# Performance work log

Measured on AMD Instinct MI355X. Metric: run time of the kernel, lower is better.

## Reference

```python
import jax, jax.numpy as jnp
import numpy as np

N = 5000        # n_stocks (nodes)
F = 128         # n_features
H = 4           # attention heads
C = 32          # hidden_size per head
HC = H * C      # GAT output dim = GRU input dim
GH = 256        # gru_hidden_size
E = 320000      # directed edges (before self-loops)
NEG_SLOPE = 0.2 # GATv2Conv default leaky_relu slope


def setup_inputs() -> dict:
    key = jax.random.key(0)
    ks = jax.random.split(key, 16)
    s = 0.05
    return {
        "x": jax.random.normal(ks[0], (N, F), dtype=jnp.float32),
        "edge_index": jax.random.randint(ks[1], (2, E), 0, N, dtype=jnp.int64),
        # GATv2Conv params (lin_l, lin_r with bias, attention vector, output bias)
        "W_l": jax.random.normal(ks[2], (F, HC), dtype=jnp.float32) * s,
        "b_l": jax.random.normal(ks[3], (HC,), dtype=jnp.float32) * s,
        "W_r": jax.random.normal(ks[4], (F, HC), dtype=jnp.float32) * s,
        "b_r": jax.random.normal(ks[5], (HC,), dtype=jnp.float32) * s,
        "att": jax.random.normal(ks[6], (H, C), dtype=jnp.float32) * s,
        "gat_bias": jax.random.normal(ks[7], (HC,), dtype=jnp.float32) * s,
        # GRU params (single layer, PyTorch gate order r,z,n)
        "W_ih": jax.random.normal(ks[8], (3 * GH, HC), dtype=jnp.float32) * s,
        "W_hh": jax.random.normal(ks[9], (3 * GH, GH), dtype=jnp.float32) * s,
        "b_ih": jax.random.normal(ks[10], (3 * GH,), dtype=jnp.float32) * s,
        "b_hh": jax.random.normal(ks[11], (3 * GH,), dtype=jnp.float32) * s,
        # policy head + log_std param
        "Wp": jax.random.normal(ks[12], (N, GH), dtype=jnp.float32) * s,
        "bp": jax.random.normal(ks[13], (N,), dtype=jnp.float32) * s,
        "log_std": jnp.zeros((N,), dtype=jnp.float32),
    }


def reference(x, edge_index, W_l, b_l, W_r, b_r, att, gat_bias,
              W_ih, W_hh, b_ih, b_hh, Wp, bp, log_std):
    # --- GATv2Conv (add_self_loops=True, concat heads, eval mode -> no dropout) ---
    loop = jnp.arange(N, dtype=edge_index.dtype)
    src = jnp.concatenate([edge_index[0], loop])  # message source j
    dst = jnp.concatenate([edge_index[1], loop])  # message target i

    xl = (x @ W_l + b_l).reshape(N, H, C)  # source-side transform
    xr = (x @ W_r + b_r).reshape(N, H, C)  # target-side transform

    m = xl[src] + xr[dst]                                  # [Etot, H, C]
    e = jnp.einsum('ehc,hc->eh', jax.nn.leaky_relu(m, NEG_SLOPE), att)

    # segment softmax over incoming edges per target node
    emax = jax.ops.segment_max(e, dst, num_segments=N)      # [N, H]
    ex = jnp.exp(e - emax[dst])
    denom = jax.ops.segment_sum(ex, dst, num_segments=N)    # [N, H]
    alpha = ex / denom[dst]                                 # [Etot, H]

    agg = jax.ops.segment_sum(alpha[:, :, None] * xl[src], dst, num_segments=N)
    gat_out = agg.reshape(N, HC) + gat_bias                 # [N, H*C]

    # --- GRU: each node = one batch element, seq_len=1, h0 = 0 ---
    gi = gat_out @ W_ih.T + b_ih                            # [N, 3*GH]
    gr, gz, gn = jnp.split(gi, 3, axis=1)
    hr, hz, hn = jnp.split(b_hh, 3)                          # h0=0 -> only hh bias
    r = jax.nn.sigmoid(gr + hr)
    z = jax.nn.sigmoid(gz + hz)
    n = jnp.tanh(gn + r * hn)
    h = (1.0 - z) * n                                        # [N, GH]

    # --- policy head ---
    mean = h @ Wp.T + bp                                     # [N, N]
    std = jnp.exp(jnp.clip(log_std, -10.0, 2.0))             # [N]
    return mean, std
```

## Files before the change

### kernel.cpp

```cpp
#include <hip/hip_runtime.h>
#include <hip/hip_bf16.h>
#include <float.h>

#define N_NODES 5000
#define F_IN    128
#define HC      128
#define GH      256
#define NE      320000
#define NET     325000
#define MPAD    5120
#define CAP     160
#define LIN_BLKS   313
#define DEC_BLKS  1270
#define NTHR    (DEC_BLKS * 256)

typedef __bf16 bf16;
typedef __attribute__((ext_vector_type(4))) __bf16 bf16x4;
typedef __attribute__((ext_vector_type(8))) __bf16 bf16x8;
typedef __attribute__((ext_vector_type(4))) float  f32x4;

__device__ __forceinline__ float lrelu(float v) { return v > 0.f ? v : 0.2f * v; }
__device__ __forceinline__ float sigm(float v) { return 1.f / (1.f + __expf(-v)); }

__device__ __forceinline__ void gload16(const void* g, void* l) {
  __builtin_amdgcn_global_load_lds((const __attribute__((address_space(1))) void*)g,
                                   (__attribute__((address_space(3))) void*)l, 16, 0, 0);
}

__global__ void k_init(int* __restrict__ cnt) {
  int i = blockIdx.x * 256 + threadIdx.x;
  if (i < N_NODES) cnt[i] = 0;
}

#define NWIH (768 * HC)
#define NWP  (N_NODES * GH)
__global__ __launch_bounds__(256) void k_pre(
    const float* __restrict__ x,
    const float* __restrict__ Wl, const float* __restrict__ bl,
    const float* __restrict__ Wr, const float* __restrict__ br,
    bf16* __restrict__ xlb, bf16* __restrict__ xrb,
    const float* __restrict__ lstd, float* __restrict__ out_std,
    const int* __restrict__ ei, int* __restrict__ cnt, int* __restrict__ csr_s,
    const float* __restrict__ wih, const float* __restrict__ wp,
    bf16* __restrict__ wihb, bf16* __restrict__ wpb) {
  __shared__ float xs[16][F_IN];
  int t = threadIdx.x;
  if (blockIdx.x < LIN_BLKS) {
    int nb = blockIdx.x * 16;
#pragma unroll
    for (int p = 0; p < 8; ++p) {
      int idx = p * 256 + t;
      int nl = idx >> 7, c = idx & 127;
      int gn = nb + nl;
      xs[nl][c] = (gn < N_NODES) ? x[(size_t)gn * F_IN + c] : 0.f;
    }
    __syncthreads();
    int col = t & 127;
    const float* W = (t < 128) ? Wl : Wr;
    float bias = (t < 128) ? bl[col] : br[col];
    float acc[16];
#pragma unroll
    for (int m = 0; m < 16; ++m) acc[m] = bias;
#pragma unroll 4
    for (int k = 0; k < F_IN; ++k) {
      float w = W[k * HC + col];
#pragma unroll
      for (int m = 0; m < 16; ++m) acc[m] = fmaf(xs[m][k], w, acc[m]);
    }
    bf16* out = (t < 128) ? xlb : xrb;
#pragma unroll
    for (int m = 0; m < 16; ++m) {
      int gn = nb + m;
      if (gn < N_NODES) out[(size_t)gn * HC + col] = (bf16)acc[m];
    }
    if (t < 16) {
      int gn = nb + t;
      if (gn < N_NODES) out_std[gn] = expf(fminf(fmaxf(lstd[gn], -10.f), 2.f));
    }
    return;
  }
  __shared__ int mode;
  if (t == 0) {
    int f = 0;
    for (int q = 1; q < 128; q += 2) f |= ei[q];
    mode = (f == 0) ? 1 : 0;
  }
  __syncthreads();
  int e = (blockIdx.x - LIN_BLKS) * 256 + t;
  for (int i = e; i < NWIH / 4; i += NTHR) {
    float4 v = reinterpret_cast<const float4*>(wih)[i];
    bf16x4 o = {(bf16)v.x, (bf16)v.y, (bf16)v.z, (bf16)v.w};
    *reinterpret_cast<bf16x4*>(&wihb[i * 4]) = o;
  }
  for (int i = e; i < NWP / 4; i += NTHR) {
    float4 v = reinterpret_cast<const float4*>(wp)[i];
    bf16x4 o = {(bf16)v.x, (bf16)v.y, (bf16)v.z, (bf16)v.w};
    *reinterpret_cast<bf16x4*>(&wpb[i * 4]) = o;
  }
  if (e >= NET) return;
  int s, d;
  if (e >= NE) { s = d = e - NE; }
  else if (mode) {
    int2 sv = *reinterpret_cast<const int2*>(&ei[2 * e]);
    int2 dv = *reinterpret_cast<const int2*>(&ei[2 * (NE + e)]);
    s = sv.x; d = dv.x;
  } else { s = ei[e]; d = ei[NE + e]; }
  int slot = atomicAdd(&cnt[d], 1);
  if (slot < CAP) csr_s[d * CAP + slot] = s;
}

__global__ __launch_bounds__(256) void k_gat(
    const bf16* __restrict__ xlb, const bf16* __restrict__ xrb,
    const int* __restrict__ csr_s, const int* __restrict__ cnt,
    const float* __restrict__ att, const float* __restrict__ gbias,
    bf16* __restrict__ gat_b) {
  int t = threadIdx.x;
  int lane = t & 63;
  int node = blockIdx.x * 4 + (t >> 6);
  if (node >= N_NODES) return;
  int c8 = lane & 15;
  int eg = lane >> 4;
  bf16x8 xr8 = *reinterpret_cast<const bf16x8*>(xrb + (size_t)node * HC + c8 * 8);
  float4 w0 = reinterpret_cast<const float4*>(att)[c8 * 2];
  float4 w1 = reinterpret_cast<const float4*>(att)[c8 * 2 + 1];
  float xr[8], wv[8];
#pragma unroll
  for (int k = 0; k < 8; ++k) xr[k] = (float)xr8[k];
  wv[0] = w0.x; wv[1] = w0.y; wv[2] = w0.z; wv[3] = w0.w;
  wv[4] = w1.x; wv[5] = w1.y; wv[6] = w1.z; wv[7] = w1.w;

  float acc[8] = {0.f, 0.f, 0.f, 0.f, 0.f, 0.f, 0.f, 0.f};
  float den = 0.f;
  int deg = cnt[node];
  deg = deg < CAP ? deg : CAP;
  int beg = node * CAP, end = node * CAP + deg;
#pragma unroll 2
  for (int p0 = beg; p0 < end; p0 += 4) {
    int p = p0 + eg;
    bool valid = p < end;
    int j = valid ? csr_s[p] : node;
    bf16x8 a8 = *reinterpret_cast<const bf16x8*>(xlb + (size_t)j * HC + c8 * 8);
    float av[8];
    float tt = 0.f;
#pragma unroll
    for (int k = 0; k < 8; ++k) {
      av[k] = (float)a8[k];
      tt = fmaf(lrelu(av[k] + xr[k]), wv[k], tt);
    }
    tt += __shfl_xor(tt, 1);
    tt += __shfl_xor(tt, 2);
    float pe = valid ? __expf(tt) : 0.f;
    den += pe;
#pragma unroll
    for (int k = 0; k < 8; ++k) acc[k] = fmaf(pe, av[k], acc[k]);
  }
#pragma unroll
  for (int m = 16; m <= 32; m <<= 1) {
    den += __shfl_xor(den, m);
#pragma unroll
    for (int k = 0; k < 8; ++k) acc[k] += __shfl_xor(acc[k], m);
  }
  if (eg == 0) {
    float4 g0 = reinterpret_cast<const float4*>(gbias)[c8 * 2];
    float4 g1 = reinterpret_cast<const float4*>(gbias)[c8 * 2 + 1];
    float gb[8] = {g0.x, g0.y, g0.z, g0.w, g1.x, g1.y, g1.z, g1.w};
    float rden = 1.f / den;
    bf16x8 o;
#pragma unroll
    for (int k = 0; k < 8; ++k) o[k] = (bf16)(acc[k] * rden + gb[k]);
    *reinterpret_cast<bf16x8*>(gat_b + (size_t)node * HC + c8 * 8) = o;
  }
}

__global__ __launch_bounds__(256) void k_gemm_gru(
    const bf16* __restrict__ A, const bf16* __restrict__ wihb,
    const float* __restrict__ bih, const float* __restrict__ bhh,
    bf16* __restrict__ hb) {
  __shared__ char smem[73728];
  char* Ab = smem;
  int t = threadIdx.x;
  int lane = t & 63, wave = t >> 6;
  int wm = wave >> 1, wn = wave & 1;
  int r16 = lane & 15, kg = lane >> 4;
  int sw7 = r16 & 7;
  int bm = blockIdx.x >> 1, bn = blockIdx.x & 1;
  int r0 = bm * 32, c0 = bn * 128;

#pragma unroll
  for (int q = 0; q < 2; ++q) {
    int idx = q * 256 + t;
    int half = idx >> 8, ih = idx & 255;
    int row = ih >> 3, cc = ih & 7;
    int gc = cc ^ (row & 7);
    gload16(&A[(size_t)(r0 + row) * 128 + half * 64 + gc * 8],
            Ab + (q * 256 + wave * 64) * 16);
  }

  auto STAGE_B = [&](int gate, int buf) {
    char* Bb = smem + 8192 + buf * 32768;
#pragma unroll
    for (int q = 0; q < 8; ++q) {
      int idx = q * 256 + t;
      int half = idx >> 10, ih = idx & 1023;
      int row = ih >> 3, cc = ih & 7;
      int gc = cc ^ (row & 7);
      gload16(&wihb[(size_t)(gate * 256 + c0 + row) * 128 + half * 64 + gc * 8],
              Bb + (q * 256 + wave * 64) * 16);
    }
  };

  int rowA = (wm * 16 + r16) * 128;
  int rowB[4];
#pragma unroll
  for (int n = 0; n < 4; ++n) rowB[n] = (wn * 64 + n * 16 + r16) * 128;

  f32x4 acc[3][4] = {};
  STAGE_B(0, 0);
  __syncthreads();
#pragma unroll
  for (int g = 0; g < 3; ++g) {
    if (g < 2) STAGE_B(g + 1, (g + 1) & 1);
    const char* Bb = smem + 8192 + (g & 1) * 32768;
#pragma unroll
    for (int h = 0; h < 2; ++h)
#pragma unroll
      for (int w = 0; w < 2; ++w) {
        int ch = ((w * 4 + kg) ^ sw7) * 16;
        bf16x8 af = *reinterpret_cast<const bf16x8*>(Ab + h * 4096 + rowA + ch);
        bf16x8 bfr[4];
#pragma unroll
        for (int n = 0; n < 4; ++n)
          bfr[n] = *reinterpret_cast<const bf16x8*>(Bb + h * 16384 + rowB[n] + ch);
#pragma unroll
        for (int n = 0; n < 4; ++n)
          acc[g][n] = __builtin_amdgcn_mfma_f32_16x16x32_bf16(af, bfr[n], acc[g][n], 0, 0, 0);
      }
    __syncthreads();
  }

  bf16* hl = (bf16*)Ab;
#pragma unroll
  for (int n = 0; n < 4; ++n) {
    int c = c0 + wn * 64 + n * 16 + r16;
    float bihr = bih[c],       bhhr = bhh[c];
    float bihz = bih[256 + c], bhhz = bhh[256 + c];
    float bihn = bih[512 + c], bhhn = bhh[512 + c];
#pragma unroll
    for (int rr = 0; rr < 4; ++rr) {
      float rg = sigm(acc[0][n][rr] + bihr + bhhr);
      float zg = sigm(acc[1][n][rr] + bihz + bhhz);
      float ng = tanhf(acc[2][n][rr] + bihn + rg * bhhn);
      float hv = (1.f - zg) * ng;
      int row = wm * 16 + kg * 4 + rr;
      hl[row * 128 + (wn * 64 + n * 16 + r16)] = (bf16)hv;
    }
  }
  __syncthreads();
#pragma unroll
  for (int q = 0; q < 2; ++q) {
    int idx = q * 256 + t;
    int row = idx >> 4, cc = idx & 15;
    *reinterpret_cast<int4*>(&hb[(size_t)(r0 + row) * GH + c0 + cc * 8]) =
        *reinterpret_cast<const int4*>(&hl[row * 128 + cc * 8]);
  }
}

__global__ __launch_bounds__(256) void gemm_nt_f32out(
    const bf16* __restrict__ A, const bf16* __restrict__ B,
    const float* __restrict__ bias, float* __restrict__ Cout,
    int K, int ldc, int Mstore, int Nstore, int nbx) {
  __shared__ char smem[65536];
  int t = threadIdx.x;
  int lane = t & 63, wave = t >> 6;
  int wm = wave >> 1, wn = wave & 1;
  int r16 = lane & 15, kg = lane >> 4;

  int wg = blockIdx.x;
  int xcd = wg & 7, i = wg >> 3;
  int bm0 = (xcd * 5 + i % 5) * 128;
  int bn0 = (i / 5) * 128;

  int rsub = lane >> 3;
  int cchk = lane & 7;

  auto STAGE = [&](int buf, int k0) {
    char* Ab = smem + buf * 32768;
#pragma unroll
    for (int q = 0; q < 4; ++q) {
      int row = (wave * 4 + q) * 8 + rsub;
      int gc = cchk ^ (row & 7);
      char* db = Ab + (wave * 4 + q) * 1024;
      gload16(&A[(size_t)(bm0 + row) * K + k0 + gc * 8], db);
      gload16(&B[(size_t)(bn0 + row) * K + k0 + gc * 8], db + 16384);
    }
  };

  f32x4 acc[4][4] = {};
  int rbA[4], rbB[4];
#pragma unroll
  for (int m = 0; m < 4; ++m) rbA[m] = (wm * 64 + m * 16 + r16) * 128;
#pragma unroll
  for (int n = 0; n < 4; ++n) rbB[n] = (wn * 64 + n * 16 + r16) * 128;
  int sw7 = r16 & 7;

  int nt = K >> 6;
  STAGE(0, 0);
  __syncthreads();
  for (int tt = 0; tt < nt; ++tt) {
    if (tt + 1 < nt) STAGE((tt & 1) ^ 1, (tt + 1) * 64);
    const char* Ab = smem + (tt & 1) * 32768;
    const char* Bb = Ab + 16384;
#pragma unroll
    for (int ks = 0; ks < 2; ++ks) {
      int ch = ((ks * 4 + kg) ^ sw7) * 16;
      bf16x8 af[4], bfr[4];
#pragma unroll
      for (int m = 0; m < 4; ++m)
        af[m] = *reinterpret_cast<const bf16x8*>(Ab + rbA[m] + ch);
#pragma unroll
      for (int n = 0; n < 4; ++n)
        bfr[n] = *reinterpret_cast<const bf16x8*>(Bb + rbB[n] + ch);
#pragma unroll
      for (int m = 0; m < 4; ++m)
#pragma unroll
        for (int n = 0; n < 4; ++n)
          acc[m][n] = __builtin_amdgcn_mfma_f32_16x16x32_bf16(af[m], bfr[n], acc[m][n], 0, 0, 0);
    }
    __syncthreads();
  }

  float bv[4];
#pragma unroll
  for (int n = 0; n < 4; ++n) {
    int gcol = bn0 + wn * 64 + n * 16 + r16;
    bv[n] = (gcol < Nstore) ? bias[gcol] : 0.f;
  }

  float* Cs = (float*)smem;
#pragma unroll
  for (int m = 0; m < 4; ++m) {
    int rb = wm * 64 + m * 16 + kg * 4;
#pragma unroll
    for (int n = 0; n < 4; ++n) {
      int cb = wn * 64 + n * 16 + r16;
#pragma unroll
      for (int r = 0; r < 4; ++r)
        Cs[(rb + r) * 128 + cb] = acc[m][n][r] + bv[n];
    }
  }
  __syncthreads();
#pragma unroll
  for (int i2 = 0; i2 < 16; ++i2) {
    int chunk = i2 * 256 + t;
    int row = chunk >> 5, cc = chunk & 31;
    int grow = bm0 + row, gcol = bn0 + cc * 4;
    if (grow < Mstore && gcol < Nstore)
      *reinterpret_cast<f32x4*>(&Cout[(size_t)grow * ldc + gcol]) =
          *reinterpret_cast<const f32x4*>(&Cs[row * 128 + cc * 4]);
  }
}

extern "C" void kernel_launch(void* const* d_in, const int* in_sizes, int n_in,
                              void* d_out, int out_size, void* d_ws, size_t ws_size,
                              hipStream_t stream) {
  const float* x     = (const float*)d_in[0];
  const int*   ei    = (const int*)d_in[1];
  const float* Wl    = (const float*)d_in[2];
  const float* bl    = (const float*)d_in[3];
  const float* Wr    = (const float*)d_in[4];
  const float* br    = (const float*)d_in[5];
  const float* att   = (const float*)d_in[6];
  const float* gbias = (const float*)d_in[7];
  const float* Wih   = (const float*)d_in[8];
  const float* bih   = (const float*)d_in[10];
  const float* bhh   = (const float*)d_in[11];
  const float* Wp    = (const float*)d_in[12];
  const float* bp    = (const float*)d_in[13];
  const float* lstd  = (const float*)d_in[14];
  float* out_mean = (float*)d_out;
  float* out_std  = out_mean + (size_t)N_NODES * N_NODES;

  char* w = (char*)d_ws;
  auto carve = [&](size_t bytes) {
    char* p = w; w += (bytes + 255) & ~(size_t)255; return p;
  };
  bf16*  xlb   = (bf16*)carve((size_t)N_NODES * HC * 2);
  bf16*  xrb   = (bf16*)carve((size_t)N_NODES * HC * 2);
  int*   cnt   = (int*)carve((size_t)N_NODES * 4);
  int*   csr_s = (int*)carve((size_t)N_NODES * CAP * 4);
  bf16*  gatb  = (bf16*)carve((size_t)MPAD * HC * 2);
  bf16*  wihb  = (bf16*)carve((size_t)768 * HC * 2);
  bf16*  hb    = (bf16*)carve((size_t)MPAD * GH * 2);
  bf16*  wpb   = (bf16*)carve((size_t)MPAD * GH * 2);

  k_init<<<(N_NODES + 255) / 256, 256, 0, stream>>>(cnt);
  k_pre<<<LIN_BLKS + DEC_BLKS, 256, 0, stream>>>(
      x, Wl, bl, Wr, br, xlb, xrb, lstd, out_std,
      ei, cnt, csr_s, Wih, Wp, wihb, wpb);
  k_gat<<<(N_NODES + 3) / 4, 256, 0, stream>>>(xlb, xrb, csr_s, cnt, att, gbias, gatb);
  k_gemm_gru<<<320, 256, 0, stream>>>(gatb, wihb, bih, bhh, hb);
  gemm_nt_f32out<<<40 * 40, 256, 0, stream>>>(hb, wpb, bp, out_mean, 256, N_NODES, N_NODES, N_NODES, 40);
}
```

Before: 100.3 us.

## Make final GEMM persistent with cross-tile prefetch and direct register stores

The final 5000x5000 policy-head GEMM now launches 512 persistent blocks instead of 1600, each looping over up to four output tiles. The K-loop double buffering runs across tile boundaries, so the next tile's first K-slice loads while the current tile finishes. The LDS-staged coalesced epilogue is dropped in favour of scalar global stores straight from the accumulators. This removes the per-tile block launch, prologue and epilogue sync, but the scalar stores are uncoalesced (16 columns per row fragment) and may raise write cost on a 100MB fp32 output.

```diff
diff --git a/kernel.cpp b/kernel.cpp
--- a/kernel.cpp
+++ b/kernel.cpp
@@ -268,22 +268,29 @@
 __global__ __launch_bounds__(256) void gemm_nt_f32out(
     const bf16* __restrict__ A, const bf16* __restrict__ B,
     const float* __restrict__ bias, float* __restrict__ Cout,
-    int K, int ldc, int Mstore, int Nstore, int nbx) {
+    int K, int ldc, int Mstore, int Nstore) {
   __shared__ char smem[65536];
   int t = threadIdx.x;
   int lane = t & 63, wave = t >> 6;
   int wm = wave >> 1, wn = wave & 1;
   int r16 = lane & 15, kg = lane >> 4;
-
-  int wg = blockIdx.x;
-  int xcd = wg & 7, i = wg >> 3;
-  int bm0 = (xcd * 5 + i % 5) * 128;
-  int bn0 = (i / 5) * 128;
-
+  int sw7 = r16 & 7;
   int rsub = lane >> 3;
   int cchk = lane & 7;
 
-  auto STAGE = [&](int buf, int k0) {
+  int bid = blockIdx.x;
+  int xcd = bid & 7, lid = bid >> 3;
+
+  int js[4]; int ntiles = 0;
+#pragma unroll
+  for (int it = 0; it < 4; ++it) {
+    int j = lid + 64 * it;
+    if (j < 200) js[ntiles++] = j;
+  }
+
+  auto STAGE = [&](int buf, int j, int k0) {
+    int bm0 = (xcd * 5 + j % 5) * 128;
+    int bn0 = (j / 5) * 128;
     char* Ab = smem + buf * 32768;
 #pragma unroll
     for (int q = 0; q < 4; ++q) {
@@ -301,14 +308,15 @@
   for (int m = 0; m < 4; ++m) rbA[m] = (wm * 64 + m * 16 + r16) * 128;
 #pragma unroll
   for (int n = 0; n < 4; ++n) rbB[n] = (wn * 64 + n * 16 + r16) * 128;
-  int sw7 = r16 & 7;
-
-  int nt = K >> 6;
-  STAGE(0, 0);
+
+  int nsteps = ntiles * 4;
+  STAGE(0, js[0], 0);
   __syncthreads();
-  for (int tt = 0; tt < nt; ++tt) {
-    if (tt + 1 < nt) STAGE((tt & 1) ^ 1, (tt + 1) * 64);
-    const char* Ab = smem + (tt & 1) * 32768;
+  int buf = 0;
+  for (int g = 0; g < nsteps; ++g) {
+    int gn = g + 1;
+    if (gn < nsteps) STAGE(buf ^ 1, js[gn >> 2], (gn & 3) * 64);
+    const char* Ab = smem + buf * 32768;
     const char* Bb = Ab + 16384;
 #pragma unroll
     for (int ks = 0; ks < 2; ++ks) {
@@ -327,36 +335,33 @@
           acc[m][n] = __builtin_amdgcn_mfma_f32_16x16x32_bf16(af[m], bfr[n], acc[m][n], 0, 0, 0);
     }
     __syncthreads();
-  }
-
-  float bv[4];
-#pragma unroll
-  for (int n = 0; n < 4; ++n) {
-    int gcol = bn0 + wn * 64 + n * 16 + r16;
-    bv[n] = (gcol < Nstore) ? bias[gcol] : 0.f;
-  }
-
-  float* Cs = (float*)smem;
-#pragma unroll
-  for (int m = 0; m < 4; ++m) {
-    int rb = wm * 64 + m * 16 + kg * 4;
-#pragma unroll
-    for (int n = 0; n < 4; ++n) {
-      int cb = wn * 64 + n * 16 + r16;
-#pragma unroll
-      for (int r = 0; r < 4; ++r)
-        Cs[(rb + r) * 128 + cb] = acc[m][n][r] + bv[n];
-    }
-  }
-  __syncthreads();
-#pragma unroll
-  for (int i2 = 0; i2 < 16; ++i2) {
-    int chunk = i2 * 256 + t;
-    int row = chunk >> 5, cc = chunk & 31;
-    int grow = bm0 + row, gcol = bn0 + cc * 4;
-    if (grow < Mstore && gcol < Nstore)
-      *reinterpret_cast<f32x4*>(&Cout[(size_t)grow * ldc + gcol]) =
-          *reinterpret_cast<const f32x4*>(&Cs[row * 128 + cc * 4]);
+    buf ^= 1;
+    if ((g & 3) == 3) {
+      int j = js[g >> 2];
+      int bm0 = (xcd * 5 + j % 5) * 128;
+      int bn0 = (j / 5) * 128;
+#pragma unroll
+      for (int n = 0; n < 4; ++n) {
+        int gcol = bn0 + wn * 64 + n * 16 + r16;
+        if (gcol < Nstore) {
+          float bv = bias[gcol];
+#pragma unroll
+          for (int m = 0; m < 4; ++m) {
+            int rowb = bm0 + wm * 64 + m * 16 + kg * 4;
+#pragma unroll
+            for (int r = 0; r < 4; ++r) {
+              int grow = rowb + r;
+              if (grow < Mstore)
+                Cout[(size_t)grow * ldc + gcol] = acc[m][n][r] + bv;
+            }
+            acc[m][n] = (f32x4){0.f, 0.f, 0.f, 0.f};
+          }
+        } else {
+#pragma unroll
+          for (int m = 0; m < 4; ++m) acc[m][n] = (f32x4){0.f, 0.f, 0.f, 0.f};
+        }
+      }
+    }
   }
 }
 
@@ -399,5 +404,5 @@
       ei, cnt, csr_s, Wih, Wp, wihb, wpb);
   k_gat<<<(N_NODES + 3) / 4, 256, 0, stream>>>(xlb, xrb, csr_s, cnt, att, gbias, gatb);
   k_gemm_gru<<<320, 256, 0, stream>>>(gatb, wihb, bih, bhh, hb);
-  gemm_nt_f32out<<<40 * 40, 256, 0, stream>>>(hb, wpb, bp, out_mean, 256, N_NODES, N_NODES, N_NODES, 40);
-}
+  gemm_nt_f32out<<<512, 256, 0, stream>>>(hb, wpb, bp, out_mean, 256, N_NODES, N_NODES, N_NODES);
+}
```

Result: slower. 120.9 us (+20.5%).
